# Performance work log

Hardware: AMD Instinct MI355X
Metric: run time of the kernel (lower is better)

## Reference

```python
import jax, jax.numpy as jnp
import numpy as np

N = 50000      # num nodes (genes)
E = 800000     # num edges (TF->Target)
IN = 128       # in_channels
HID = 16       # hidden_channels per head
HEADS = 4
OUT = 32       # out_channels
NEG_SLOPE = 0.2  # PyG GATConv leaky_relu slope
EPS = 1e-16


def setup_inputs() -> dict:
    key = jax.random.key(0)
    ks = jax.random.split(key, 11)
    x = jax.random.normal(ks[0], (N, IN), dtype=jnp.float32)
    edge_index = jax.random.randint(ks[1], (2, E), 0, N, dtype=jnp.int32)
    # layer 1: heads=HEADS, concat=True
    W1 = jax.random.normal(ks[2], (IN, HEADS * HID), dtype=jnp.float32) * (1.0 / np.sqrt(IN))
    a_src1 = jax.random.normal(ks[3], (HEADS, HID), dtype=jnp.float32) * 0.1
    a_dst1 = jax.random.normal(ks[4], (HEADS, HID), dtype=jnp.float32) * 0.1
    b1 = jnp.zeros((HEADS * HID,), dtype=jnp.float32)
    # layer 2: heads=1, concat=False
    W2 = jax.random.normal(ks[5], (HEADS * HID, OUT), dtype=jnp.float32) * (1.0 / np.sqrt(HEADS * HID))
    a_src2 = jax.random.normal(ks[6], (1, OUT), dtype=jnp.float32) * 0.1
    a_dst2 = jax.random.normal(ks[7], (1, OUT), dtype=jnp.float32) * 0.1
    b2 = jnp.zeros((OUT,), dtype=jnp.float32)
    return dict(x=x, edge_index=edge_index, W1=W1, a_src1=a_src1, a_dst1=a_dst1, b1=b1,
                W2=W2, a_src2=a_src2, a_dst2=a_dst2, b2=b2)


def gat_layer(x, edge_index, W, a_src, a_dst, b, concat):
    """PyG GATConv (no self-loops, eval mode): gather -> edge attention -> segment softmax -> scatter."""
    n = x.shape[0]
    heads, ch = a_src.shape
    h = (x @ W).reshape(n, heads, ch)                      # [N, H, C]
    alpha_s = jnp.einsum('nhc,hc->nh', h, a_src)           # [N, H]
    alpha_d = jnp.einsum('nhc,hc->nh', h, a_dst)           # [N, H]
    src, dst = edge_index[0], edge_index[1]
    e = jax.nn.leaky_relu(alpha_s[src] + alpha_d[dst], negative_slope=NEG_SLOPE)  # [E, H]
    # numerically stable softmax over incoming edges of each dst node
    m = jax.ops.segment_max(e, dst, num_segments=n)        # [N, H]
    e = jnp.exp(e - m[dst])
    denom = jax.ops.segment_sum(e, dst, num_segments=n)    # [N, H]
    alpha = e / (denom[dst] + EPS)                         # [E, H]
    msg = h[src] * alpha[:, :, None]                       # [E, H, C]
    out = jax.ops.segment_sum(msg, dst, num_segments=n)    # [N, H, C]
    if concat:
        out = out.reshape(n, heads * ch)
    else:
        out = out.mean(axis=1)
    return out + b


def reference(x, edge_index, W1, a_src1, a_dst1, b1, W2, a_src2, a_dst2, b2):
    h = gat_layer(x, edge_index, W1, a_src1, a_dst1, b1, concat=True)   # [N, HEADS*HID]
    h = jax.nn.elu(h)
    out = gat_layer(h, edge_index, W2, a_src2, a_dst2, b2, concat=False)  # [N, OUT]
    return out
```

## Files before the change

### kernel.cpp

```cpp
#include <hip/hip_runtime.h>
#include <hip/hip_fp16.h>
#include <math.h>

#define NN 50000
#define NE 800000
#define INCH 128
#define HID1 16
#define H1 4
#define C1 64
#define C2 32
#define NEG 0.2f
#define EPSF 1e-16f
#define CAP 128
#define BSH 7
#define NBKT 391
#define CAPB 3072
#define EPB 2048
#define NPB1 391
#define GB1 782
#define POISON 0xAAAAAAAAu

static __device__ __forceinline__ float lrelu(float v){ return v > 0.f ? v : NEG * v; }


__global__ __launch_bounds__(256) void k_part1(
        const int* __restrict__ ei, unsigned* bcnt, unsigned* __restrict__ pairs,
        const float* __restrict__ x, const float* __restrict__ W,
        const float* __restrict__ asrc, const float* __restrict__ adst,
        __half* __restrict__ h, float* __restrict__ as1, float* __restrict__ ad1){
    __shared__ __align__(16) char smem[76288];
    int t = threadIdx.x;

    if (blockIdx.x < NPB1){
        int* hist = (int*)smem;
        int* scn  = (int*)(smem + 2048);
        int* spos = (int*)(smem + 4096);
        unsigned* gbase = (unsigned*)(smem + 6144);
        unsigned* stg   = (unsigned*)(smem + 7708);
        hist[t] = 0; hist[t + 256] = 0;
        __syncthreads();

        int e0 = blockIdx.x * EPB;
        int tot = NE - e0; if (tot > EPB) tot = EPB;
        unsigned pk[8]; int rnk[8], bkt[8];
        #pragma unroll
        for (int k = 0; k < 8; ++k){
            int idx = k * 256 + t;
            if (idx < tot){
                int e = e0 + idx;
                int s = ei[e];
                int d = ei[NE + e];
                bkt[k] = d >> BSH;
                pk[k] = ((unsigned)bkt[k] << 23) | ((unsigned)(d & 127) << 16) | (unsigned)s;
                rnk[k] = atomicAdd(&hist[bkt[k]], 1);
            } else bkt[k] = -1;
        }
        __syncthreads();

        int* sA = hist; int* sB = scn;
        for (int off = 1; off < 512; off <<= 1){
            int v0 = sA[t]       + ((t       >= off) ? sA[t - off]       : 0);
            int v1 = sA[t + 256] + ((t + 256 >= off) ? sA[t + 256 - off] : 0);
            __syncthreads();
            sB[t] = v0; sB[t + 256] = v1;
            __syncthreads();
            int* tmp = sA; sA = sB; sB = tmp;
        }
        for (int b = t; b < NBKT; b += 256){
            int incl = sA[b];
            int excl = (b > 0) ? sA[b - 1] : 0;
            spos[b] = excl;
            int cnt = incl - excl;
            unsigned off = 0;
            if (cnt > 0){
                unsigned old = atomicAdd(&bcnt[b], (unsigned)cnt);
                off = old - POISON;
                if (off > (unsigned)(CAPB - cnt)) off = 0;
            }
            gbase[b] = off;
        }
        __syncthreads();

        #pragma unroll
        for (int k = 0; k < 8; ++k)
            if (bkt[k] >= 0)
                stg[spos[bkt[k]] + rnk[k]] = pk[k];
        __syncthreads();

        for (int i = t; i < tot; i += 256){
            unsigned v = stg[i];
            int b = v >> 23;
            pairs[b * CAPB + gbase[b] + (i - spos[b])] = v;
        }
    } else {
        float (*XT)[68] = (float(*)[68])smem;
        float* WS = (float*)(smem + 34816);
        float (*ps)[17] = (float(*)[17])(smem + 67584);
        float (*pd)[17] = (float(*)[17])(smem + 71936);
        int bid = blockIdx.x - NPB1;

        int nodeL = t >> 2;
        int kc = t & 3;
        int g = bid * 64 + nodeL;
        int gc = min(g, NN - 1);
        const float4* xr = (const float4*)(x + (size_t)gc * INCH);
        #pragma unroll
        for (int i = 0; i < 8; ++i){
            int k = kc * 32 + i * 4;
            float4 v = xr[k >> 2];
            XT[k + 0][nodeL] = v.x;
            XT[k + 1][nodeL] = v.y;
            XT[k + 2][nodeL] = v.z;
            XT[k + 3][nodeL] = v.w;
        }
        const float4* W4 = (const float4*)W;
        float4* WS4 = (float4*)WS;
        #pragma unroll
        for (int i = 0; i < 8; ++i) WS4[i * 256 + t] = W4[i * 256 + t];
        __syncthreads();

        int tx = t & 15, ty = t >> 4;
        int c4 = tx * 4, n4 = ty * 4;
        float acc[4][4];
        #pragma unroll
        for (int a = 0; a < 4; ++a)
            #pragma unroll
            for (int b2 = 0; b2 < 4; ++b2) acc[a][b2] = 0.f;

        #pragma unroll 8
        for (int k = 0; k < INCH; ++k){
            float4 xa = *(const float4*)&XT[k][n4];
            float4 wb = *(const float4*)&WS[k * C1 + c4];
            const float xv[4] = {xa.x, xa.y, xa.z, xa.w};
            const float wv[4] = {wb.x, wb.y, wb.z, wb.w};
            #pragma unroll
            for (int a = 0; a < 4; ++a)
                #pragma unroll
                for (int b2 = 0; b2 < 4; ++b2)
                    acc[a][b2] = fmaf(xv[a], wv[b2], acc[a][b2]);
        }

        int hd = tx >> 2;
        #pragma unroll
        for (int a = 0; a < 4; ++a){
            int n = bid * 64 + n4 + a;
            if (n < NN){
                union { __half2 q[2]; float2 f; } u;
                u.q[0] = __floats2half2_rn(acc[a][0], acc[a][1]);
                u.q[1] = __floats2half2_rn(acc[a][2], acc[a][3]);
                *(float2*)&h[n * C1 + c4] = u.f;
            }
            float sa = 0.f, da = 0.f;
            #pragma unroll
            for (int b2 = 0; b2 < 4; ++b2){
                sa = fmaf(acc[a][b2], asrc[hd * HID1 + (c4 & 15) + b2], sa);
                da = fmaf(acc[a][b2], adst[hd * HID1 + (c4 & 15) + b2], da);
            }
            ps[n4 + a][tx] = sa;
            pd[n4 + a][tx] = da;
        }
        __syncthreads();
        int nd = t & 63, hh = t >> 6;
        int g2 = bid * 64 + nd;
        if (g2 < NN){
            float sa = ps[nd][hh*4+0] + ps[nd][hh*4+1] + ps[nd][hh*4+2] + ps[nd][hh*4+3];
            float da = pd[nd][hh*4+0] + pd[nd][hh*4+1] + pd[nd][hh*4+2] + pd[nd][hh*4+3];
            as1[g2 * H1 + hh] = sa;
            ad1[g2 * H1 + hh] = da;
        }
    }
}


__global__ __launch_bounds__(256) void k_build2(
        const unsigned* __restrict__ pairs, const unsigned* __restrict__ bcnt,
        int* __restrict__ rows, int* __restrict__ deg, int* __restrict__ srcs){
    __shared__ __align__(16) char smem[13824];
    int t = threadIdx.x;

    unsigned* stg = (unsigned*)smem;
    int* hist = (int*)(smem + 12288);
    int* scn  = (int*)(smem + 12800);
    int* cur  = (int*)(smem + 13312);
    int b = blockIdx.x;
    int n0 = b << BSH;
    unsigned cntu = bcnt[b] - POISON;
    if (cntu > (unsigned)CAPB) cntu = (b == NBKT - 1) ? 0u : (unsigned)CAPB;
    int cnt = (int)cntu;
    if (t < 128) hist[t] = 0;
    __syncthreads();
    const unsigned* psrc = pairs + b * CAPB;
    for (int i = t; i < cnt; i += 256){
        unsigned v = psrc[i];
        stg[i] = v;
        atomicAdd(&hist[(v >> 16) & 127], 1);
    }
    __syncthreads();
    int v = (t < 128) ? hist[t] : 0;
    if (t < 128) scn[t] = v;
    __syncthreads();
    for (int off = 1; off < 128; off <<= 1){
        int add = (t < 128 && t >= off) ? scn[t - off] : 0;
        __syncthreads();
        if (t < 128) scn[t] += add;
        __syncthreads();
    }
    if (t < 128){
        int base = b * CAPB + (scn[t] - v);
        cur[t] = base;
        int n = n0 + t;
        if (n < NN){ rows[n] = base; deg[n] = v; }
    }
    __syncthreads();
    for (int i = t; i < cnt; i += 256){
        unsigned pv = stg[i];
        int p = atomicAdd(&cur[(pv >> 16) & 127], 1);
        srcs[p] = (int)(pv & 0xFFFFu);
    }
}


__global__ __launch_bounds__(256) void k_aggA(
        const int* __restrict__ srcs, const int* __restrict__ rows,
        const int* __restrict__ deg, const __half* __restrict__ h1,
        const float* __restrict__ as, const float* __restrict__ ad,
        const float* __restrict__ b1, const float* __restrict__ W2,
        const float* __restrict__ a2s, const float* __restrict__ a2d,
        __half* __restrict__ h2, float* __restrict__ as2, float* __restrict__ ad2){
    __shared__ float vbuf[4][H1][132];
    __shared__ int   sbuf[4][CAP];
    __shared__ float hpT[4][68];
    int t = threadIdx.x;
    int w = t >> 6, lane = t & 63;
    int hd1 = lane & 3, eb = lane >> 2;
    int node = blockIdx.x * 4 + w;
    int start = rows[node], dg = deg[node];

    if (dg <= CAP){
        int dgp = (dg + 15) & ~15;
        for (int j = lane; j < dgp; j += 64)
            sbuf[w][j] = (j < dg) ? srcs[start + j] : 0;

        int hd2 = lane >> 4;
        const __half* hc = h1 + lane;
        __half hv[16];
        #pragma unroll
        for (int k = 0; k < 16; ++k)
            hv[k] = hc[sbuf[w][k] * C1];

        float adv = ad[node * H1 + hd1];
        float ssum = 0.f;
        for (int j = eb; j < dg; j += 16){
            int s = sbuf[w][j];
            float wv = __expf(lrelu(as[s * H1 + hd1] + adv));
            vbuf[w][hd1][j] = wv;
            ssum += wv;
        }
        if (lane < dgp - dg){
            int j = dg + lane;
            vbuf[w][0][j] = 0.f; vbuf[w][1][j] = 0.f;
            vbuf[w][2][j] = 0.f; vbuf[w][3][j] = 0.f;
        }
        ssum += __shfl_xor(ssum, 4);
        ssum += __shfl_xor(ssum, 8);
        ssum += __shfl_xor(ssum, 16);
        ssum += __shfl_xor(ssum, 32);
        float inv = 1.f / (__shfl(ssum, hd2) + EPSF);

        const float* wrow = vbuf[w][hd2];
        float a0 = 0.f, a1 = 0.f, a2 = 0.f, a3 = 0.f;
        #pragma unroll
        for (int k = 0; k < 16; k += 4){
            a0 = fmaf(__half2float(hv[k + 0]), wrow[k + 0], a0);
            a1 = fmaf(__half2float(hv[k + 1]), wrow[k + 1], a1);
            a2 = fmaf(__half2float(hv[k + 2]), wrow[k + 2], a2);
            a3 = fmaf(__half2float(hv[k + 3]), wrow[k + 3], a3);
        }
        for (int j0 = 16; j0 < dgp; j0 += 16){
            #pragma unroll
            for (int k = 0; k < 16; ++k)
                hv[k] = hc[sbuf[w][j0 + k] * C1];
            #pragma unroll
            for (int k = 0; k < 16; k += 4){
                a0 = fmaf(__half2float(hv[k + 0]), wrow[j0 + k + 0], a0);
                a1 = fmaf(__half2float(hv[k + 1]), wrow[j0 + k + 1], a1);
                a2 = fmaf(__half2float(hv[k + 2]), wrow[j0 + k + 2], a2);
                a3 = fmaf(__half2float(hv[k + 3]), wrow[j0 + k + 3], a3);
            }
        }
        float o = ((a0 + a1) + (a2 + a3)) * inv + b1[lane];
        hpT[w][lane] = o > 0.f ? o : (__expf(o) - 1.f);
    } else {
        int hdf = lane >> 4;
        float adv = ad[node * H1 + hdf];
        float ss = 0.f, ac = 0.f;
        for (int j = 0; j < dg; ++j){
            int s = srcs[start + j];
            float wv = __expf(lrelu(as[s * H1 + hdf] + adv));
            ss += wv;
            ac = fmaf(__half2float(h1[s * C1 + lane]), wv, ac);
        }
        float o = ac / (ss + EPSF) + b1[lane];
        hpT[w][lane] = o > 0.f ? o : (__expf(o) - 1.f);
    }

    int c = lane & 31, k0 = (lane >> 5) * 32;
    const float* W2c = W2 + c;
    float a = 0.f;
    #pragma unroll
    for (int kk = 0; kk < 32; kk += 4){
        float4 hv4 = *(const float4*)&hpT[w][k0 + kk];
        a = fmaf(hv4.x, W2c[(k0 + kk) * C2], a);
        a = fmaf(hv4.y, W2c[(k0 + kk + 1) * C2], a);
        a = fmaf(hv4.z, W2c[(k0 + kk + 2) * C2], a);
        a = fmaf(hv4.w, W2c[(k0 + kk + 3) * C2], a);
    }
    a += __shfl_xor(a, 32);
    int gn = blockIdx.x * 4 + w;
    if ((lane >> 5) == 0){
        h2[gn * C2 + c] = __float2half(a);
        float sa = a * a2s[c];
        float da = a * a2d[c];
        #pragma unroll
        for (int off = 16; off >= 1; off >>= 1){
            sa += __shfl_xor(sa, off);
            da += __shfl_xor(da, off);
        }
        if (c == 0){ as2[gn] = sa; ad2[gn] = da; }
    }
}


__global__ __launch_bounds__(256) void k_agg2(
        const int* __restrict__ srcs, const int* __restrict__ rows,
        const int* __restrict__ deg, const __half* __restrict__ h2,
        const float* __restrict__ as, const float* __restrict__ ad,
        const float* __restrict__ b2, float* __restrict__ out){
    __shared__ float vbuf[8][CAP];
    __shared__ int   sbuf[8][CAP];
    int sl = threadIdx.x >> 5;
    int lane = threadIdx.x & 31;
    int node = blockIdx.x * 8 + sl;
    int start = rows[node], dg = deg[node];
    float adv = ad[node];

    if (dg <= CAP){
        int dgp = (dg + 15) & ~15;
        for (int j = lane; j < dgp; j += 32)
            sbuf[sl][j] = (j < dg) ? srcs[start + j] : 0;

        const __half* hc = h2 + lane;
        __half hv[16];
        #pragma unroll
        for (int k = 0; k < 16; ++k)
            hv[k] = hc[sbuf[sl][k] * C2];

        float ssum = 0.f;
        for (int j = lane; j < dg; j += 32){
            int s = sbuf[sl][j];
            float wv = __expf(lrelu(as[s] + adv));
            vbuf[sl][j] = wv;
            ssum += wv;
        }
        if (lane < dgp - dg) vbuf[sl][dg + lane] = 0.f;
        #pragma unroll
        for (int off = 1; off < 32; off <<= 1) ssum += __shfl_xor(ssum, off);
        float inv = 1.f / (ssum + EPSF);

        const float* wrow = vbuf[sl];
        float a0 = 0.f, a1 = 0.f, a2 = 0.f, a3 = 0.f;
        #pragma unroll
        for (int k = 0; k < 16; k += 4){
            a0 = fmaf(__half2float(hv[k + 0]), wrow[k + 0], a0);
            a1 = fmaf(__half2float(hv[k + 1]), wrow[k + 1], a1);
            a2 = fmaf(__half2float(hv[k + 2]), wrow[k + 2], a2);
            a3 = fmaf(__half2float(hv[k + 3]), wrow[k + 3], a3);
        }
        for (int j0 = 16; j0 < dgp; j0 += 16){
            #pragma unroll
            for (int k = 0; k < 16; ++k)
                hv[k] = hc[sbuf[sl][j0 + k] * C2];
            #pragma unroll
            for (int k = 0; k < 16; k += 4){
                a0 = fmaf(__half2float(hv[k + 0]), wrow[j0 + k + 0], a0);
                a1 = fmaf(__half2float(hv[k + 1]), wrow[j0 + k + 1], a1);
                a2 = fmaf(__half2float(hv[k + 2]), wrow[j0 + k + 2], a2);
                a3 = fmaf(__half2float(hv[k + 3]), wrow[j0 + k + 3], a3);
            }
        }
        out[node * C2 + lane] = ((a0 + a1) + (a2 + a3)) * inv + b2[lane];
    } else {
        float ss = 0.f, ac = 0.f;
        for (int j = 0; j < dg; ++j){
            int s = srcs[start + j];
            float wv = __expf(lrelu(as[s] + adv));
            ss += wv;
            ac = fmaf(__half2float(h2[s * C2 + lane]), wv, ac);
        }
        out[node * C2 + lane] = ac / (ss + EPSF) + b2[lane];
    }
}

extern "C" void kernel_launch(void* const* d_in, const int* in_sizes, int n_in,
                              void* d_out, int out_size, void* d_ws, size_t ws_size,
                              hipStream_t stream) {
    const float* x    = (const float*)d_in[0];
    const int*   ei   = (const int*)  d_in[1];
    const float* W1   = (const float*)d_in[2];
    const float* as1w = (const float*)d_in[3];
    const float* ad1w = (const float*)d_in[4];
    const float* b1   = (const float*)d_in[5];
    const float* W2   = (const float*)d_in[6];
    const float* as2w = (const float*)d_in[7];
    const float* ad2w = (const float*)d_in[8];
    const float* b2   = (const float*)d_in[9];
    float* out = (float*)d_out;

    float* p = (float*)d_ws;
    __half* h1 = (__half*)p; p += (size_t)NN * C1 / 2;
    __half* h2 = (__half*)p; p += (size_t)NN * C2 / 2;
    float* as1  = p; p += (size_t)NN * H1;
    float* ad1  = p; p += (size_t)NN * H1;
    float* as2  = p; p += NN;
    float* ad2  = p; p += NN;
    int* deg  = (int*)p; p += NN;
    int* rows = (int*)p; p += NN;
    unsigned* bcnt = (unsigned*)p; p += NBKT + 57;
    int* srcs = (int*)p; p += (size_t)NBKT * CAPB;
    unsigned* pairs = (unsigned*)p;

    dim3 B(256);
    k_part1 <<<NPB1 + GB1, B, 0, stream>>>(ei, bcnt, pairs,
                                           x, W1, as1w, ad1w, h1, as1, ad1);
    k_build2<<<NBKT, B, 0, stream>>>(pairs, bcnt, rows, deg, srcs);
    k_aggA  <<<NN / 4, B, 0, stream>>>(srcs, rows, deg, h1, as1, ad1, b1,
                                       W2, as2w, ad2w, h2, as2, ad2);
    k_agg2  <<<NN / 8, B, 0, stream>>>(srcs, rows, deg, h2, as2, ad2, b2, out);
}
```

Measured before the change: 173.9 us.

## Split layer-2 projection into separate tiled kernel and shrink part1 LDS footprint

The per-node W2 projection is moved out of the aggregation kernel into a new k_h2 kernel. The aggregation kernel now writes the ELU output to a float32 workspace, and k_h2 does the 128-node tiled matmul with W2 held in LDS. Separately, the layer-1 GEMM in k_part1 now streams x in four 32-row chunks instead of staging the full transposed tile. The per-head attention reduction now uses shuffles instead of an LDS pass. Together these cut shared memory from about 76 KB to about 41 KB to raise occupancy, in exchange for an extra kernel launch and a 12.8 MB float round trip through global memory.

```diff
diff --git a/kernel.cpp b/kernel.cpp
--- a/kernel.cpp
+++ b/kernel.cpp
@@ -28,7 +28,7 @@
         const float* __restrict__ x, const float* __restrict__ W,
         const float* __restrict__ asrc, const float* __restrict__ adst,
         __half* __restrict__ h, float* __restrict__ as1, float* __restrict__ ad1){
-    __shared__ __align__(16) char smem[76288];
+    __shared__ __align__(16) char smem[41472];
     int t = threadIdx.x;
 
     if (blockIdx.x < NPB1){
@@ -93,31 +93,20 @@
             pairs[b * CAPB + gbase[b] + (i - spos[b])] = v;
         }
     } else {
-        float (*XT)[68] = (float(*)[68])smem;
-        float* WS = (float*)(smem + 34816);
-        float (*ps)[17] = (float(*)[17])(smem + 67584);
-        float (*pd)[17] = (float(*)[17])(smem + 71936);
+        float* WS = (float*)smem;
+        float (*XTc)[68] = (float(*)[68])(smem + 32768);
         int bid = blockIdx.x - NPB1;
+
+        const float4* W4 = (const float4*)W;
+        float4* WS4 = (float4*)WS;
+        #pragma unroll
+        for (int i = 0; i < 8; ++i) WS4[i * 256 + t] = W4[i * 256 + t];
 
         int nodeL = t >> 2;
         int kc = t & 3;
         int g = bid * 64 + nodeL;
         int gc = min(g, NN - 1);
         const float4* xr = (const float4*)(x + (size_t)gc * INCH);
-        #pragma unroll
-        for (int i = 0; i < 8; ++i){
-            int k = kc * 32 + i * 4;
-            float4 v = xr[k >> 2];
-            XT[k + 0][nodeL] = v.x;
-            XT[k + 1][nodeL] = v.y;
-            XT[k + 2][nodeL] = v.z;
-            XT[k + 3][nodeL] = v.w;
-        }
-        const float4* W4 = (const float4*)W;
-        float4* WS4 = (float4*)WS;
-        #pragma unroll
-        for (int i = 0; i < 8; ++i) WS4[i * 256 + t] = W4[i * 256 + t];
-        __syncthreads();
 
         int tx = t & 15, ty = t >> 4;
         int c4 = tx * 4, n4 = ty * 4;
@@ -127,17 +116,29 @@
             #pragma unroll
             for (int b2 = 0; b2 < 4; ++b2) acc[a][b2] = 0.f;
 
-        #pragma unroll 8
-        for (int k = 0; k < INCH; ++k){
-            float4 xa = *(const float4*)&XT[k][n4];
-            float4 wb = *(const float4*)&WS[k * C1 + c4];
-            const float xv[4] = {xa.x, xa.y, xa.z, xa.w};
-            const float wv[4] = {wb.x, wb.y, wb.z, wb.w};
-            #pragma unroll
-            for (int a = 0; a < 4; ++a)
+        for (int ch = 0; ch < 4; ++ch){
+            __syncthreads();
+            float4 v0 = xr[ch * 8 + kc * 2 + 0];
+            float4 v1 = xr[ch * 8 + kc * 2 + 1];
+            int kb = kc * 8;
+            XTc[kb + 0][nodeL] = v0.x; XTc[kb + 1][nodeL] = v0.y;
+            XTc[kb + 2][nodeL] = v0.z; XTc[kb + 3][nodeL] = v0.w;
+            XTc[kb + 4][nodeL] = v1.x; XTc[kb + 5][nodeL] = v1.y;
+            XTc[kb + 6][nodeL] = v1.z; XTc[kb + 7][nodeL] = v1.w;
+            __syncthreads();
+            const float* Wc = WS + ch * 32 * C1;
+            #pragma unroll 8
+            for (int k = 0; k < 32; ++k){
+                float4 xa = *(const float4*)&XTc[k][n4];
+                float4 wb = *(const float4*)&Wc[k * C1 + c4];
+                const float xv[4] = {xa.x, xa.y, xa.z, xa.w};
+                const float wv[4] = {wb.x, wb.y, wb.z, wb.w};
                 #pragma unroll
-                for (int b2 = 0; b2 < 4; ++b2)
-                    acc[a][b2] = fmaf(xv[a], wv[b2], acc[a][b2]);
+                for (int a = 0; a < 4; ++a)
+                    #pragma unroll
+                    for (int b2 = 0; b2 < 4; ++b2)
+                        acc[a][b2] = fmaf(xv[a], wv[b2], acc[a][b2]);
+            }
         }
 
         int hd = tx >> 2;
@@ -156,17 +157,12 @@
                 sa = fmaf(acc[a][b2], asrc[hd * HID1 + (c4 & 15) + b2], sa);
                 da = fmaf(acc[a][b2], adst[hd * HID1 + (c4 & 15) + b2], da);
             }
-            ps[n4 + a][tx] = sa;
-            pd[n4 + a][tx] = da;
-        }
-        __syncthreads();
-        int nd = t & 63, hh = t >> 6;
-        int g2 = bid * 64 + nd;
-        if (g2 < NN){
-            float sa = ps[nd][hh*4+0] + ps[nd][hh*4+1] + ps[nd][hh*4+2] + ps[nd][hh*4+3];
-            float da = pd[nd][hh*4+0] + pd[nd][hh*4+1] + pd[nd][hh*4+2] + pd[nd][hh*4+3];
-            as1[g2 * H1 + hh] = sa;
-            ad1[g2 * H1 + hh] = da;
+            sa += __shfl_xor(sa, 1); sa += __shfl_xor(sa, 2);
+            da += __shfl_xor(da, 1); da += __shfl_xor(da, 2);
+            if ((tx & 3) == 0 && n < NN){
+                as1[n * H1 + hd] = sa;
+                ad1[n * H1 + hd] = da;
+            }
         }
     }
 }
@@ -224,12 +220,9 @@
         const int* __restrict__ srcs, const int* __restrict__ rows,
         const int* __restrict__ deg, const __half* __restrict__ h1,
         const float* __restrict__ as, const float* __restrict__ ad,
-        const float* __restrict__ b1, const float* __restrict__ W2,
-        const float* __restrict__ a2s, const float* __restrict__ a2d,
-        __half* __restrict__ h2, float* __restrict__ as2, float* __restrict__ ad2){
+        const float* __restrict__ b1, float* __restrict__ hp){
     __shared__ float vbuf[4][H1][132];
     __shared__ int   sbuf[4][CAP];
-    __shared__ float hpT[4][68];
     int t = threadIdx.x;
     int w = t >> 6, lane = t & 63;
     int hd1 = lane & 3, eb = lane >> 2;
@@ -289,7 +282,7 @@
             }
         }
         float o = ((a0 + a1) + (a2 + a3)) * inv + b1[lane];
-        hpT[w][lane] = o > 0.f ? o : (__expf(o) - 1.f);
+        hp[(size_t)node * C1 + lane] = o > 0.f ? o : (__expf(o) - 1.f);
     } else {
         int hdf = lane >> 4;
         float adv = ad[node * H1 + hdf];
@@ -301,32 +294,66 @@
             ac = fmaf(__half2float(h1[s * C1 + lane]), wv, ac);
         }
         float o = ac / (ss + EPSF) + b1[lane];
-        hpT[w][lane] = o > 0.f ? o : (__expf(o) - 1.f);
-    }
-
-    int c = lane & 31, k0 = (lane >> 5) * 32;
-    const float* W2c = W2 + c;
-    float a = 0.f;
+        hp[(size_t)node * C1 + lane] = o > 0.f ? o : (__expf(o) - 1.f);
+    }
+}
+
+
+__global__ __launch_bounds__(256) void k_h2(
+        const float* __restrict__ hp, const float* __restrict__ W2,
+        const float* __restrict__ a2s, const float* __restrict__ a2d,
+        __half* __restrict__ h2, float* __restrict__ as2, float* __restrict__ ad2){
+    __shared__ float W2s[C1 * C2];
+    __shared__ float tile[128][66];
+    int t = threadIdx.x;
+    int n0 = blockIdx.x * 128;
+
+    const float4* w4 = (const float4*)W2;
+    float4* ws4 = (float4*)W2s;
+    ws4[t] = w4[t];
+    ws4[t + 256] = w4[t + 256];
+
+    const float4* hp4 = (const float4*)hp;
     #pragma unroll
-    for (int kk = 0; kk < 32; kk += 4){
-        float4 hv4 = *(const float4*)&hpT[w][k0 + kk];
-        a = fmaf(hv4.x, W2c[(k0 + kk) * C2], a);
-        a = fmaf(hv4.y, W2c[(k0 + kk + 1) * C2], a);
-        a = fmaf(hv4.z, W2c[(k0 + kk + 2) * C2], a);
-        a = fmaf(hv4.w, W2c[(k0 + kk + 3) * C2], a);
-    }
-    a += __shfl_xor(a, 32);
-    int gn = blockIdx.x * 4 + w;
-    if ((lane >> 5) == 0){
-        h2[gn * C2 + c] = __float2half(a);
-        float sa = a * a2s[c];
-        float da = a * a2d[c];
-        #pragma unroll
-        for (int off = 16; off >= 1; off >>= 1){
-            sa += __shfl_xor(sa, off);
-            da += __shfl_xor(da, off);
-        }
-        if (c == 0){ as2[gn] = sa; ad2[gn] = da; }
+    for (int i = 0; i < 8; ++i){
+        int idx = i * 256 + t;
+        int r = idx >> 4;
+        int c4 = (idx & 15) << 2;
+        int gn = n0 + r; if (gn >= NN) gn = NN - 1;
+        float4 v = hp4[(size_t)gn * 16 + (idx & 15)];
+        tile[r][c4 + 0] = v.x; tile[r][c4 + 1] = v.y;
+        tile[r][c4 + 2] = v.z; tile[r][c4 + 3] = v.w;
+    }
+    __syncthreads();
+
+    int n = t >> 1, hf = t & 1;
+    int gn = n0 + n;
+    float acc[16];
+    #pragma unroll
+    for (int c = 0; c < 16; ++c) acc[c] = 0.f;
+    #pragma unroll 4
+    for (int k = 0; k < C1; ++k){
+        float hv = tile[n][k];
+        const float* wk = W2s + k * C2 + hf * 16;
+        #pragma unroll
+        for (int c = 0; c < 16; ++c) acc[c] = fmaf(hv, wk[c], acc[c]);
+    }
+    float sa = 0.f, da = 0.f;
+    #pragma unroll
+    for (int c = 0; c < 16; ++c){
+        sa = fmaf(acc[c], a2s[hf * 16 + c], sa);
+        da = fmaf(acc[c], a2d[hf * 16 + c], da);
+    }
+    sa += __shfl_xor(sa, 1);
+    da += __shfl_xor(da, 1);
+    if (gn < NN){
+        union { __half2 q[8]; float4 f[2]; } u;
+        #pragma unroll
+        for (int c2 = 0; c2 < 8; ++c2)
+            u.q[c2] = __floats2half2_rn(acc[2 * c2], acc[2 * c2 + 1]);
+        *(float4*)&h2[(size_t)gn * C2 + hf * 16]     = u.f[0];
+        *(float4*)&h2[(size_t)gn * C2 + hf * 16 + 8] = u.f[1];
+        if (hf == 0){ as2[gn] = sa; ad2[gn] = da; }
     }
 }
 
@@ -419,6 +446,7 @@
     float* p = (float*)d_ws;
     __half* h1 = (__half*)p; p += (size_t)NN * C1 / 2;
     __half* h2 = (__half*)p; p += (size_t)NN * C2 / 2;
+    float* hp  = p; p += (size_t)NN * C1;
     float* as1  = p; p += (size_t)NN * H1;
     float* ad1  = p; p += (size_t)NN * H1;
     float* as2  = p; p += NN;
@@ -433,7 +461,7 @@
     k_part1 <<<NPB1 + GB1, B, 0, stream>>>(ei, bcnt, pairs,
                                            x, W1, as1w, ad1w, h1, as1, ad1);
     k_build2<<<NBKT, B, 0, stream>>>(pairs, bcnt, rows, deg, srcs);
-    k_aggA  <<<NN / 4, B, 0, stream>>>(srcs, rows, deg, h1, as1, ad1, b1,
-                                       W2, as2w, ad2w, h2, as2, ad2);
+    k_aggA  <<<NN / 4, B, 0, stream>>>(srcs, rows, deg, h1, as1, ad1, b1, hp);
+    k_h2    <<<NBKT, B, 0, stream>>>(hp, W2, as2w, ad2w, h2, as2, ad2);
     k_agg2  <<<NN / 8, B, 0, stream>>>(srcs, rows, deg, h2, as2, ad2, b2, out);
 }
```

Result: no change. 170.6 us (-1.9%).
